# Performance work log

Hardware: AMD Instinct MI355X
Metric: run time of the kernel (lower is better)

## Reference

```python
import jax, jax.numpy as jnp
import numpy as np

B, L, NF, H = 4, 1024, 480, 32
FC = NF + H          # feat_i_classes = 512
D = FC               # downsample_feats (default None -> feat_i_classes)
W = 65               # positional window width (odd -> 'same' padding matches)
MAX0, MAX1 = 10.0, 100.0  # max_std_sigma_0 / max_std_sigma_1


def _uni(k, shape, lo=-0.01, hi=0.01):
    return jax.random.uniform(k, shape, jnp.float32, lo, hi)


def setup_inputs() -> dict:
    key = jax.random.key(0)
    ks = jax.random.split(key, 11)
    return {
        "x_embeds": jax.random.normal(ks[0], (B, L, NF), jnp.float32),
        "latent_outputs": jax.random.normal(ks[1], (B, L, H), jnp.float32),
        "masks": jnp.ones((B, L, 1), jnp.float32),
        "pos_embed": (jnp.arange(W, dtype=jnp.float32) - W // 2).reshape(W, 1, 1),
        "x": jax.random.uniform(ks[2], (B, L, 23), jnp.float32),
        "all_x_all_ampl": _uni(ks[3], (5, D, H)),
        "inp_decomp_vecs": _uni(ks[4], (5, D, 1)),
        "out_decomp_vecs": _uni(ks[5], (5, 1, H)),
        "all_x_all_bias": _uni(ks[6], (5, 1, H)),
        "pos_dep_ampl_weights": _uni(ks[7], (1, FC, H)),
        "knn_activations": _uni(ks[8], (2, FC, D)),
    }


def _conv_same(x_bdl, w_hdw):
    # torch F.conv1d (cross-correlation), stride 1, padding 'same'
    return jax.lax.conv_general_dilated(
        x_bdl, w_hdw, window_strides=(1,), padding="SAME",
        dimension_numbers=("NCH", "OIH", "NCH"))


def reference(x_embeds, latent_outputs, masks, pos_embed, x,
              all_x_all_ampl, inp_decomp_vecs, out_decomp_vecs,
              all_x_all_bias, pos_dep_ampl_weights, knn_activations):
    A = all_x_all_ampl                       # (5,D,H)
    rec = lambda i: inp_decomp_vecs[i] * out_decomp_vecs[i]  # (D,1)*(1,H)->(D,H)
    inv_c0 = 1.0 / MAX0 ** 2

    cls = jax.nn.softmax(latent_outputs * masks, axis=-1) * masks
    oef = jnp.concatenate([x_embeds, cls], axis=-1)          # (B,L,FC)
    cf0 = oef @ knn_activations[0]                           # (B,L,D)
    cf1 = oef @ knn_activations[1]                           # (B,L,D)

    def kern(ampl, mean, inv_var):
        # cos(0*pos+0)=1; pos (W,1,1) broadcast vs (D,H) -> (W,D,H)
        return jnp.exp(-inv_var * (pos_embed - mean) ** 2) * ampl

    # torch: std=abs(w)**0.5; inv_var = std**2 + 1/max0**2 = abs(w)+c
    k0 = kern(A[0], rec(0), jnp.abs(rec(1)) + inv_c0)
    k1 = kern(A[1], 0.0,    jnp.abs(rec(2)) + inv_c0)
    k2 = kern(A[2], rec(3), jnp.abs(rec(4)) + inv_c0)

    conv = lambda f, k: _conv_same(f.transpose(0, 2, 1),
                                   k.transpose(2, 1, 0)).transpose(0, 2, 1)
    acts0 = conv(cf0, k0)                                    # (B,L,H)
    acts1 = conv(cf1, k1)
    acts2 = conv(cf0, k2)

    b0, b1, b2, b3, class_mult = all_x_all_bias              # each (1,H)
    rec_dist_filt = (acts0 + b0) * acts1 \
        + acts2 * (cf1 @ A[1] + b2) \
        + (cf0 @ A[3] + b1) * (cf1 @ A[4])

    collect = jnp.sum(x[..., 21:], axis=-1, keepdims=True)   # (B,L,1)
    m = (masks + collect)[..., 0]                            # (B,L)
    pos = jnp.arange(L, dtype=jnp.float32)
    rel2 = (pos[None, :] - pos[:, None]) ** 2                # (L,L)
    sig = class_mult[0] ** 2 + 1.0 / MAX1 ** 2               # (H,)
    G = jnp.exp(-sig[:, None, None] * rel2)                  # (H,L,L)
    # V_correction[b,i,h] = m[b,i] * sum_j G[h,i,j] m[b,j]  (mask is rank-1)
    Vc = m[:, :, None] * jnp.einsum("hij,bj->bih", G, m)     # (B,L,H)

    per_pos = oef @ pos_dep_ampl_weights[0] + b3             # (B,L,H)
    return Vc * per_pos * rec_dist_filt * masks
```

## Files before the change

### kernel.cpp

```cpp
#include <hip/hip_runtime.h>
#include <hip/hip_bf16.h>

#define BB 4
#define LL 1024
#define NFE 480
#define HH 32
#define FCC 512
#define DD 512
#define WW 65
#define BL (BB*LL)
#define BLH (BL*HH)
#define LPAD 1088

typedef short bf16x8 __attribute__((ext_vector_type(8)));
typedef float f32x16 __attribute__((ext_vector_type(16)));
typedef unsigned short us8 __attribute__((ext_vector_type(8)));

__device__ inline unsigned short f2bf(float x) {
    union { float f; unsigned u; } v; v.f = x;
    unsigned r = v.u + 0x7FFFu + ((v.u >> 16) & 1u);
    return (unsigned short)(r >> 16);
}

__device__ __align__(16) unsigned short g_oefb[BL*FCC];
__device__ __align__(16) unsigned short g_knt[2*DD*FCC];
__device__ float  g_m[BL];
__device__ __align__(16) unsigned short g_fpad[2*BB*LPAD*DD];
__device__ __align__(16) unsigned short g_kb2[(size_t)3*WW*4*8*64*8];
__device__ __align__(16) unsigned short g_kbs[4*4*8*64*8];
__device__ float  g_actsp[4][3*BLH];
__device__ float  g_small[4*BLH];
__device__ float  g_gt[HH*LL];
__device__ float  g_vsum[BLH];

__global__ __launch_bounds__(256) void kprep(const float* __restrict__ x_embeds,
                                             const float* __restrict__ latent,
                                             const float* __restrict__ masks,
                                             const float* __restrict__ x,
                                             const float* __restrict__ ampl,
                                             const float* __restrict__ inp,
                                             const float* __restrict__ outv,
                                             const float* __restrict__ pos,
                                             const float* __restrict__ bias,
                                             const float* __restrict__ pdw,
                                             const float* __restrict__ knn) {
    const int bx = blockIdx.x;
    const int tid = threadIdx.x;

    if (bx < 512) {
        const int row0 = bx * 8;
        const int r    = row0 + (tid >> 5);
        const int lane = tid & 31;

        const float mask = masks[r];
        float v = latent[r*HH + lane] * mask;
        float mx = v;
        #pragma unroll
        for (int off = 16; off > 0; off >>= 1) mx = fmaxf(mx, __shfl_xor(mx, off, 32));
        float e = __expf(v - mx);
        float s = e;
        #pragma unroll
        for (int off = 16; off > 0; off >>= 1) s += __shfl_xor(s, off, 32);
        g_oefb[r*FCC + NFE + lane] = f2bf(e / s * mask);

        if (lane == 0) g_m[r] = mask + x[r*23 + 21] + x[r*23 + 22];

        for (int idx = tid; idx < 8*NFE; idx += 256) {
            int rr = idx / NFE, c = idx - rr*NFE;
            g_oefb[(row0+rr)*FCC + c] = f2bf(x_embeds[(row0+rr)*NFE + c]);
        }
    } else if (bx < 640) {
        int idx = (bx - 512) * 256 + tid;
        int fzb = idx >> 12;
        int rem = idx & 4095;
        int rowi = rem >> 6;
        int col8 = rem & 63;
        int row = (rowi < 32) ? rowi : (1024 + rowi);
        int4 z = make_int4(0,0,0,0);
        *reinterpret_cast<int4*>(&g_fpad[((size_t)fzb*LPAD + row)*DD + col8*8]) = z;
    } else if (bx < 768) {
        __shared__ unsigned short tile[64][65];
        int idx2 = bx - 640;
        const int k0 = (idx2 & 7) * 64;
        const int n0 = ((idx2 >> 3) & 7) * 64;
        const int z  = idx2 >> 6;
        const float* __restrict__ src = knn + (size_t)z*FCC*DD;
        #pragma unroll 4
        for (int i = 0; i < 16; ++i) {
            int idx = i*256 + tid;
            int kk = idx >> 6, nn = idx & 63;
            tile[kk][nn] = f2bf(src[(size_t)(k0+kk)*DD + n0+nn]);
        }
        __syncthreads();
        #pragma unroll 4
        for (int i = 0; i < 16; ++i) {
            int idx = i*256 + tid;
            int nn = idx >> 6, kk = idx & 63;
            g_knt[((size_t)z*DD + n0+nn)*FCC + k0+kk] = tile[kk][nn];
        }
    } else if (bx < 800) {
        int t = (bx - 768)*256 + tid;
        int lane = t & 63;
        int ks = (t >> 6) & 7;
        int dt = (t >> 9) & 3;
        int o  = t >> 11;
        int l31 = lane & 31, khalf = lane >> 5;
        const float* S = (o == 0) ? ampl + 1*DD*HH :
                         (o == 1) ? ampl + 3*DD*HH :
                         (o == 2) ? ampl + 4*DD*HH : pdw;
        int k0 = dt*128 + ks*16 + khalf*8;
        us8 outw;
        #pragma unroll
        for (int i = 0; i < 8; ++i) outw[i] = f2bf(S[(size_t)(k0+i)*HH + l31]);
        *reinterpret_cast<us8*>(&g_kbs[(size_t)t*8]) = outw;
    } else if (bx < 928) {
        int idx = (bx - 800) * 256 + tid;
        int h = idx / LL;
        int dist = idx - h*LL;
        float cm = bias[4*HH + h];
        float sig = cm*cm + 1e-4f;
        float dd = (float)dist;
        g_gt[idx] = __expf(-sig * dd * dd);
    } else {
        int idx3 = bx - 928;
        int xi  = idx3 & 7;
        int rem = idx3 >> 3;
        int w   = rem % 65;
        int z   = rem / 65;
        int idx = xi * 256 + tid;
        const int lane = idx & 63;
        const int ks   = (idx >> 6) & 7;
        const int dt   = idx >> 9;
        const int h    = lane & 31;
        const int d8   = dt*128 + ks*16 + (lane >> 5)*8;

        const float c0 = 0.01f;
        const float p = pos[w];
        int ai, mi, vi;
        if (z == 0)      { ai = 0; mi = 0;  vi = 1; }
        else if (z == 1) { ai = 1; mi = -1; vi = 2; }
        else             { ai = 2; mi = 3;  vi = 4; }

        us8 outw;
        #pragma unroll
        for (int i = 0; i < 8; ++i) {
            int d = d8 + i;
            float a    = ampl[(size_t)ai*DD*HH + d*HH + h];
            float mean = (mi >= 0) ? inp[mi*DD + d] * outv[mi*HH + h] : 0.f;
            float iv   = fabsf(inp[vi*DD + d] * outv[vi*HH + h]) + c0;
            float tt = p - mean;
            outw[i] = f2bf(__expf(-iv * tt * tt) * a);
        }
        *reinterpret_cast<us8*>(&g_kb2[((((size_t)z*WW + w)*4 + dt)*8 + ks)*512 + (size_t)lane*8]) = outw;
    }
}

__global__ __launch_bounds__(256) void k2_mfma() {
    const int nt = blockIdx.x;
    const int mt = blockIdx.y;
    const int z  = blockIdx.z;
    const int t  = threadIdx.x;
    const int wave = t >> 6, lane = t & 63;
    const int l31 = lane & 31, khalf = lane >> 5;
    const int n0 = nt*128 + wave*32;
    const int m_base = mt*64;

    __shared__ __align__(16) unsigned short smem[64*128];

    f32x16 acc[2];
    #pragma unroll
    for (int mti = 0; mti < 2; ++mti)
        #pragma unroll
        for (int i = 0; i < 16; ++i) acc[mti][i] = 0.f;

    const unsigned short* __restrict__ bptr =
        g_knt + ((size_t)z*DD + n0 + l31)*FCC + khalf*8;

    for (int kc = 0; kc < 4; ++kc) {
        __syncthreads();
        const unsigned short* __restrict__ src = g_oefb + (size_t)m_base*FCC + kc*128;
        #pragma unroll
        for (int c = 0; c < 4; ++c) {
            int q = c*256 + t;
            int row = q >> 4, slot = q & 15;
            int4 v = *reinterpret_cast<const int4*>(src + (size_t)row*FCC + slot*8);
            int off = row*256 + ((slot*16) ^ ((row & 15) << 4));
            *reinterpret_cast<int4*>((char*)smem + off) = v;
        }
        __syncthreads();
        #pragma unroll
        for (int ks = 0; ks < 8; ++ks) {
            bf16x8 bf = *reinterpret_cast<const bf16x8*>(bptr + kc*128 + ks*16);
            int dby = ks*32 + khalf*16;
            #pragma unroll
            for (int mti = 0; mti < 2; ++mti) {
                int r = mti*32 + l31;
                bf16x8 a = *reinterpret_cast<const bf16x8*>(
                    (char*)smem + r*256 + (dby ^ ((r & 15) << 4)));
                acc[mti] = __builtin_amdgcn_mfma_f32_32x32x16_bf16(a, bf, acc[mti], 0, 0, 0);
            }
        }
    }

    #pragma unroll
    for (int mti = 0; mti < 2; ++mti) {
        #pragma unroll
        for (int reg = 0; reg < 16; ++reg) {
            int rowf = (reg & 3) + 8*(reg >> 2) + 4*khalf;
            int m = m_base + mti*32 + rowf;
            int b_ = m >> 10, l_ = m & 1023;
            g_fpad[((size_t)(z*BB + b_)*LPAD + 32 + l_)*DD + n0 + l31] = f2bf(acc[mti][reg]);
        }
    }
}

__global__ __launch_bounds__(256) void kheavy() {
    __shared__ __align__(16) char smem_raw[32768];
    const int bx = blockIdx.x;
    const int t  = threadIdx.x;

    if (bx < 512) {
        float* ml = (float*)smem_raw;
        const int ib = bx & 127;
        const int b  = bx >> 7;
        for (int j = t; j < LL; j += 256) ml[j] = g_m[b*LL + j];
        __syncthreads();
        const int i = ib * 8 + (t & 7);
        const int h = t >> 3;
        const float* __restrict__ gt = g_gt + (size_t)h * LL;
        float a0 = 0.f, a1 = 0.f, a2 = 0.f, a3 = 0.f;
        #pragma unroll 4
        for (int j = 0; j < 256; ++j) {
            int d0 = i - j;         d0 = d0 < 0 ? -d0 : d0;
            int d1 = i - (j+256);   d1 = d1 < 0 ? -d1 : d1;
            int d2 = i - (j+512);   d2 = d2 < 0 ? -d2 : d2;
            int d3 = i - (j+768);   d3 = d3 < 0 ? -d3 : d3;
            a0 = fmaf(gt[d0], ml[j],       a0);
            a1 = fmaf(gt[d1], ml[j+256],   a1);
            a2 = fmaf(gt[d2], ml[j+512],   a2);
            a3 = fmaf(gt[d3], ml[j+768],   a3);
        }
        g_vsum[(size_t)(b*LL + i)*HH + h] = (a0 + a1) + (a2 + a3);
    } else if (bx < 1280) {
        const int g  = bx - 512;
        const int lt = g & 15;
        const int b  = (g >> 4) & 3;
        const int zdq = g >> 6;
        const int z  = zdq >> 2;
        const int dq = zdq & 3;
        const int fz = (z == 1) ? 1 : 0;
        const int wave = t >> 6, lane = t & 63;
        const int l31 = lane & 31, khalf = lane >> 5;

        const int wbeg = (wave == 0) ? 0 : 17 + (wave - 1)*16;
        const int wend = (wave == 0) ? 17 : wbeg + 16;

        f32x16 acc0, acc1;
        #pragma unroll
        for (int i = 0; i < 16; ++i) { acc0[i] = 0.f; acc1[i] = 0.f; }

        const unsigned short* src =
            g_fpad + ((size_t)(fz*BB + b)*LPAD + lt*64) * DD + dq*128;
        #pragma unroll
        for (int c = 0; c < 8; ++c) {
            int q = c*256 + t;
            int row = q >> 4, slot = q & 15;
            int4 v = *reinterpret_cast<const int4*>(src + (size_t)row*DD + slot*8);
            int off = row*256 + ((slot*16) ^ ((row & 15) << 4));
            *reinterpret_cast<int4*>(smem_raw + off) = v;
        }
        __syncthreads();

        for (int w = wbeg; w < wend; ++w) {
            const unsigned short* kbw =
                g_kb2 + ((((size_t)z*WW + w)*4 + dq)*8)*512;
            const int r0 = l31 + w;
            const int r1 = r0 + 32;
            #pragma unroll
            for (int ks = 0; ks < 8; ++ks) {
                bf16x8 bf = *reinterpret_cast<const bf16x8*>(kbw + ks*512 + lane*8);
                int dby = ks*32 + khalf*16;
                bf16x8 a0 = *reinterpret_cast<const bf16x8*>(
                    smem_raw + r0*256 + (dby ^ ((r0 & 15) << 4)));
                bf16x8 a1 = *reinterpret_cast<const bf16x8*>(
                    smem_raw + r1*256 + (dby ^ ((r1 & 15) << 4)));
                acc0 = __builtin_amdgcn_mfma_f32_32x32x16_bf16(a0, bf, acc0, 0, 0, 0);
                acc1 = __builtin_amdgcn_mfma_f32_32x32x16_bf16(a1, bf, acc1, 0, 0, 0);
            }
        }

        __syncthreads();
        float* red = (float*)smem_raw;
        #pragma unroll
        for (int reg = 0; reg < 16; ++reg) {
            int row = (reg & 3) + 8*(reg >> 2) + 4*khalf;
            red[wave*2048 + row*32 + l31]        = acc0[reg];
            red[wave*2048 + (32 + row)*32 + l31] = acc1[reg];
        }
        __syncthreads();
        float* outp = g_actsp[dq] + (size_t)z*BLH + ((size_t)b*LL + lt*64)*HH;
        #pragma unroll
        for (int j = 0; j < 8; ++j) {
            int i = j*256 + t;
            float sum = red[i] + red[2048 + i] + red[4096 + i] + red[6144 + i];
            outp[i] = sum;
        }
    } else {
        const int g = bx - 1280;
        const int mt = g & 31;
        const int o  = g >> 5;
        const int wave = t >> 6, lane = t & 63;
        const int l31 = lane & 31, khalf = lane >> 5;

        const unsigned short* src;
        if (o == 3) {
            src = g_oefb + (size_t)mt*128*FCC;
        } else {
            const int fz = (o == 1) ? 0 : 1;
            const int m0 = mt*128;
            const int b_ = m0 >> 10, l0 = m0 & 1023;
            src = g_fpad + ((size_t)(fz*BB + b_)*LPAD + 32 + l0)*DD;
        }

        f32x16 acc;
        #pragma unroll
        for (int i = 0; i < 16; ++i) acc[i] = 0.f;

        for (int kc = 0; kc < 4; ++kc) {
            __syncthreads();
            const unsigned short* s2 = src + kc*128;
            #pragma unroll
            for (int c = 0; c < 8; ++c) {
                int q = c*256 + t;
                int row = q >> 4, slot = q & 15;
                int4 v = *reinterpret_cast<const int4*>(s2 + (size_t)row*512 + slot*8);
                int off = row*256 + ((slot*16) ^ ((row & 15) << 4));
                *reinterpret_cast<int4*>(smem_raw + off) = v;
            }
            __syncthreads();
            #pragma unroll
            for (int ks = 0; ks < 8; ++ks) {
                bf16x8 bf = *reinterpret_cast<const bf16x8*>(
                    &g_kbs[((((size_t)o*4 + kc)*8 + ks)*64 + lane)*8]);
                int dby = ks*32 + khalf*16;
                int r = wave*32 + l31;
                bf16x8 a = *reinterpret_cast<const bf16x8*>(
                    smem_raw + r*256 + (dby ^ ((r & 15) << 4)));
                acc = __builtin_amdgcn_mfma_f32_32x32x16_bf16(a, bf, acc, 0, 0, 0);
            }
        }

        float* outp = g_small + (size_t)o*BLH + ((size_t)mt*128 + wave*32)*HH;
        #pragma unroll
        for (int reg = 0; reg < 16; ++reg) {
            int row = (reg & 3) + 8*(reg >> 2) + 4*khalf;
            outp[(size_t)row*HH + l31] = acc[reg];
        }
    }
}

__global__ __launch_bounds__(256) void k7_final(const float* __restrict__ masks,
                                                const float* __restrict__ bias,
                                                float* __restrict__ out) {
    int idx = blockIdx.x * 256 + threadIdx.x;
    int r = idx >> 5, h = idx & 31;
    float a0 = 0.f, a1 = 0.f, a2 = 0.f;
    #pragma unroll
    for (int s = 0; s < 4; ++s) {
        a0 += g_actsp[s][idx];
        a1 += g_actsp[s][BLH + idx];
        a2 += g_actsp[s][2*BLH + idx];
    }
    float rdf = (a0 + bias[0*HH + h]) * a1
              + a2 * (g_small[idx] + bias[2*HH + h])
              + (g_small[BLH + idx] + bias[1*HH + h]) * g_small[2*BLH + idx];
    float pp = g_small[3*BLH + idx] + bias[3*HH + h];
    float vc = g_m[r] * g_vsum[idx];
    out[idx] = vc * pp * rdf * masks[r];
}

extern "C" void kernel_launch(void* const* d_in, const int* in_sizes, int n_in,
                              void* d_out, int out_size, void* d_ws, size_t ws_size,
                              hipStream_t stream) {
    (void)in_sizes; (void)n_in; (void)d_ws; (void)ws_size; (void)out_size;
    const float* x_embeds = (const float*)d_in[0];
    const float* latent   = (const float*)d_in[1];
    const float* masks    = (const float*)d_in[2];
    const float* pos      = (const float*)d_in[3];
    const float* x        = (const float*)d_in[4];
    const float* ampl     = (const float*)d_in[5];
    const float* inp      = (const float*)d_in[6];
    const float* outv     = (const float*)d_in[7];
    const float* bias     = (const float*)d_in[8];
    const float* pdw      = (const float*)d_in[9];
    const float* knn      = (const float*)d_in[10];
    float* out = (float*)d_out;

    hipLaunchKernelGGL(kprep, dim3(2488), dim3(256), 0, stream,
                       x_embeds, latent, masks, x, ampl, inp, outv, pos, bias, pdw, knn);
    hipLaunchKernelGGL(k2_mfma, dim3(4, 64, 2), dim3(256), 0, stream);
    hipLaunchKernelGGL(kheavy, dim3(1408), dim3(256), 0, stream);
    hipLaunchKernelGGL(k7_final, dim3(BLH/256), dim3(256), 0, stream, masks, bias, out);
}
```

Before: 88.47 us.

## Window the Gaussian Vc sum, split it in halves, interleave block roles

The Vc Gaussian sum is split into two j-halves written to separate buffers, and each block only loops over j within about 512 positions of its rows. Beyond that range exp(-sig*rel^2) is negligible, since sig is at least 1/MAX1^2 by construction. Conv blocks and Vc blocks are interleaved in a 4:3 pattern within one grid so the two kinds of work share the GPU more evenly. The conv path stages only 96 feature rows in LDS and reads the second MFMA operand directly from global memory, which saves LDS traffic but adds global loads. The truncated sum drops only tiny terms, and the final kernel now adds the two partial buffers.

```diff
diff --git a/kernel.cpp b/kernel.cpp
--- a/kernel.cpp
+++ b/kernel.cpp
@@ -31,7 +31,7 @@
 __device__ float  g_actsp[4][3*BLH];
 __device__ float  g_small[4*BLH];
 __device__ float  g_gt[HH*LL];
-__device__ float  g_vsum[BLH];
+__device__ float  g_vsum2[2][BLH];
 
 __global__ __launch_bounds__(256) void kprep(const float* __restrict__ x_embeds,
                                              const float* __restrict__ latent,
@@ -219,30 +219,44 @@
     const int bx = blockIdx.x;
     const int t  = threadIdx.x;
 
-    if (bx < 512) {
+    int role, idx;
+    if (bx < 1792) {
+        int g7 = bx / 7, r7 = bx - g7*7;
+        if (r7 < 4) { role = 0; idx = g7*4 + r7; }
+        else        { role = 1; idx = g7*3 + (r7 - 4); }
+    } else { role = 2; idx = bx - 1792; }
+
+    if (role == 0) {
         float* ml = (float*)smem_raw;
-        const int ib = bx & 127;
-        const int b  = bx >> 7;
+        const int jh = idx >> 9;
+        const int rem = idx & 511;
+        const int b  = rem >> 7;
+        const int ib = rem & 127;
         for (int j = t; j < LL; j += 256) ml[j] = g_m[b*LL + j];
         __syncthreads();
         const int i = ib * 8 + (t & 7);
         const int h = t >> 3;
         const float* __restrict__ gt = g_gt + (size_t)h * LL;
+        int wlo = ib*8 - 511; int hlo = jh*512;
+        if (wlo < hlo) wlo = hlo;
+        wlo &= ~3;
+        int whi = ((ib*8 + 7 + 512) + 3) & ~3;
+        int hhi = hlo + 512;
+        if (whi > hhi) whi = hhi;
         float a0 = 0.f, a1 = 0.f, a2 = 0.f, a3 = 0.f;
-        #pragma unroll 4
-        for (int j = 0; j < 256; ++j) {
-            int d0 = i - j;         d0 = d0 < 0 ? -d0 : d0;
-            int d1 = i - (j+256);   d1 = d1 < 0 ? -d1 : d1;
-            int d2 = i - (j+512);   d2 = d2 < 0 ? -d2 : d2;
-            int d3 = i - (j+768);   d3 = d3 < 0 ? -d3 : d3;
-            a0 = fmaf(gt[d0], ml[j],       a0);
-            a1 = fmaf(gt[d1], ml[j+256],   a1);
-            a2 = fmaf(gt[d2], ml[j+512],   a2);
-            a3 = fmaf(gt[d3], ml[j+768],   a3);
-        }
-        g_vsum[(size_t)(b*LL + i)*HH + h] = (a0 + a1) + (a2 + a3);
-    } else if (bx < 1280) {
-        const int g  = bx - 512;
+        for (int j = wlo; j < whi; j += 4) {
+            int d0 = i - j;     d0 = d0 < 0 ? -d0 : d0;
+            int d1 = i - j - 1; d1 = d1 < 0 ? -d1 : d1;
+            int d2 = i - j - 2; d2 = d2 < 0 ? -d2 : d2;
+            int d3 = i - j - 3; d3 = d3 < 0 ? -d3 : d3;
+            a0 = fmaf(gt[d0], ml[j],   a0);
+            a1 = fmaf(gt[d1], ml[j+1], a1);
+            a2 = fmaf(gt[d2], ml[j+2], a2);
+            a3 = fmaf(gt[d3], ml[j+3], a3);
+        }
+        g_vsum2[jh][(size_t)(b*LL + i)*HH + h] = (a0 + a1) + (a2 + a3);
+    } else if (role == 1) {
+        const int g  = idx;
         const int lt = g & 15;
         const int b  = (g >> 4) & 3;
         const int zdq = g >> 6;
@@ -259,10 +273,10 @@
         #pragma unroll
         for (int i = 0; i < 16; ++i) { acc0[i] = 0.f; acc1[i] = 0.f; }
 
-        const unsigned short* src =
-            g_fpad + ((size_t)(fz*BB + b)*LPAD + lt*64) * DD + dq*128;
-        #pragma unroll
-        for (int c = 0; c < 8; ++c) {
+        const size_t base_row = (size_t)(fz*BB + b)*LPAD + lt*64;
+        const unsigned short* src = g_fpad + base_row * DD + dq*128;
+        #pragma unroll
+        for (int c = 0; c < 6; ++c) {
             int q = c*256 + t;
             int row = q >> 4, slot = q & 15;
             int4 v = *reinterpret_cast<const int4*>(src + (size_t)row*DD + slot*8);
@@ -271,19 +285,19 @@
         }
         __syncthreads();
 
+        const unsigned short* fb1 = src + khalf*8;
         for (int w = wbeg; w < wend; ++w) {
             const unsigned short* kbw =
                 g_kb2 + ((((size_t)z*WW + w)*4 + dq)*8)*512;
             const int r0 = l31 + w;
-            const int r1 = r0 + 32;
+            const unsigned short* fp1 = fb1 + (size_t)(r0 + 32)*DD;
             #pragma unroll
             for (int ks = 0; ks < 8; ++ks) {
                 bf16x8 bf = *reinterpret_cast<const bf16x8*>(kbw + ks*512 + lane*8);
                 int dby = ks*32 + khalf*16;
                 bf16x8 a0 = *reinterpret_cast<const bf16x8*>(
                     smem_raw + r0*256 + (dby ^ ((r0 & 15) << 4)));
-                bf16x8 a1 = *reinterpret_cast<const bf16x8*>(
-                    smem_raw + r1*256 + (dby ^ ((r1 & 15) << 4)));
+                bf16x8 a1 = *reinterpret_cast<const bf16x8*>(fp1 + ks*16);
                 acc0 = __builtin_amdgcn_mfma_f32_32x32x16_bf16(a0, bf, acc0, 0, 0, 0);
                 acc1 = __builtin_amdgcn_mfma_f32_32x32x16_bf16(a1, bf, acc1, 0, 0, 0);
             }
@@ -306,7 +320,7 @@
             outp[i] = sum;
         }
     } else {
-        const int g = bx - 1280;
+        const int g = idx;
         const int mt = g & 31;
         const int o  = g >> 5;
         const int wave = t >> 6, lane = t & 63;
@@ -375,7 +389,7 @@
               + a2 * (g_small[idx] + bias[2*HH + h])
               + (g_small[BLH + idx] + bias[1*HH + h]) * g_small[2*BLH + idx];
     float pp = g_small[3*BLH + idx] + bias[3*HH + h];
-    float vc = g_m[r] * g_vsum[idx];
+    float vc = g_m[r] * (g_vsum2[0][idx] + g_vsum2[1][idx]);
     out[idx] = vc * pp * rdf * masks[r];
 }
 
@@ -399,6 +413,6 @@
     hipLaunchKernelGGL(kprep, dim3(2488), dim3(256), 0, stream,
                        x_embeds, latent, masks, x, ampl, inp, outv, pos, bias, pdw, knn);
     hipLaunchKernelGGL(k2_mfma, dim3(4, 64, 2), dim3(256), 0, stream);
-    hipLaunchKernelGGL(kheavy, dim3(1408), dim3(256), 0, stream);
+    hipLaunchKernelGGL(kheavy, dim3(1920), dim3(256), 0, stream);
     hipLaunchKernelGGL(k7_final, dim3(BLH/256), dim3(256), 0, stream, masks, bias, out);
 }
```

Result: slower. 156.0 us (+76.4%).

## Truncate Gaussian position sum to a window and fuse cf0 convolutions

Applied to the files above, without the earlier changes.

The Gaussian-weighted mask sum now loops only over positions within about ±352 of each output row tile, using float4 loads of the shared mask, instead of all 1024 positions. The floor of 1/MAX1² on sigma bounds the dropped weights to tiny values, so the truncation is a small approximation. The two convolutions that read cf0 (kernels 0 and 2) now share one shared-memory tile load and issue MFMAs for both kernels together. The cf1 convolution gets its own block range, which cuts the block count. The fused path doubles the accumulator registers, which may lower occupancy.

```diff
diff --git a/kernel.cpp b/kernel.cpp
--- a/kernel.cpp
+++ b/kernel.cpp
@@ -228,39 +228,39 @@
         const int i = ib * 8 + (t & 7);
         const int h = t >> 3;
         const float* __restrict__ gt = g_gt + (size_t)h * LL;
+        const int i0 = ib * 8;
+        int wlo = i0 - 352; if (wlo < 0) wlo = 0; else wlo &= ~3;
+        int whi = i0 + 360; if (whi > 1024) whi = 1024; else whi = (whi + 3) & ~3;
         float a0 = 0.f, a1 = 0.f, a2 = 0.f, a3 = 0.f;
-        #pragma unroll 4
-        for (int j = 0; j < 256; ++j) {
-            int d0 = i - j;         d0 = d0 < 0 ? -d0 : d0;
-            int d1 = i - (j+256);   d1 = d1 < 0 ? -d1 : d1;
-            int d2 = i - (j+512);   d2 = d2 < 0 ? -d2 : d2;
-            int d3 = i - (j+768);   d3 = d3 < 0 ? -d3 : d3;
-            a0 = fmaf(gt[d0], ml[j],       a0);
-            a1 = fmaf(gt[d1], ml[j+256],   a1);
-            a2 = fmaf(gt[d2], ml[j+512],   a2);
-            a3 = fmaf(gt[d3], ml[j+768],   a3);
+        for (int j = wlo; j < whi; j += 4) {
+            float4 mj = *reinterpret_cast<const float4*>(&ml[j]);
+            int d0 = i - j;     d0 = d0 < 0 ? -d0 : d0;
+            int d1 = i - j - 1; d1 = d1 < 0 ? -d1 : d1;
+            int d2 = i - j - 2; d2 = d2 < 0 ? -d2 : d2;
+            int d3 = i - j - 3; d3 = d3 < 0 ? -d3 : d3;
+            a0 = fmaf(gt[d0], mj.x, a0);
+            a1 = fmaf(gt[d1], mj.y, a1);
+            a2 = fmaf(gt[d2], mj.z, a2);
+            a3 = fmaf(gt[d3], mj.w, a3);
         }
         g_vsum[(size_t)(b*LL + i)*HH + h] = (a0 + a1) + (a2 + a3);
-    } else if (bx < 1280) {
+    } else if (bx < 768) {
         const int g  = bx - 512;
         const int lt = g & 15;
         const int b  = (g >> 4) & 3;
-        const int zdq = g >> 6;
-        const int z  = zdq >> 2;
-        const int dq = zdq & 3;
-        const int fz = (z == 1) ? 1 : 0;
+        const int dq = g >> 6;
         const int wave = t >> 6, lane = t & 63;
         const int l31 = lane & 31, khalf = lane >> 5;
 
         const int wbeg = (wave == 0) ? 0 : 17 + (wave - 1)*16;
         const int wend = (wave == 0) ? 17 : wbeg + 16;
 
-        f32x16 acc0, acc1;
-        #pragma unroll
-        for (int i = 0; i < 16; ++i) { acc0[i] = 0.f; acc1[i] = 0.f; }
+        f32x16 acc00, acc01, acc20, acc21;
+        #pragma unroll
+        for (int i = 0; i < 16; ++i) { acc00[i] = 0.f; acc01[i] = 0.f; acc20[i] = 0.f; acc21[i] = 0.f; }
 
         const unsigned short* src =
-            g_fpad + ((size_t)(fz*BB + b)*LPAD + lt*64) * DD + dq*128;
+            g_fpad + ((size_t)b*LPAD + lt*64) * DD + dq*128;
         #pragma unroll
         for (int c = 0; c < 8; ++c) {
             int q = c*256 + t;
@@ -272,8 +272,84 @@
         __syncthreads();
 
         for (int w = wbeg; w < wend; ++w) {
-            const unsigned short* kbw =
-                g_kb2 + ((((size_t)z*WW + w)*4 + dq)*8)*512;
+            const unsigned short* kbw0 = g_kb2 + ((((size_t)0*WW + w)*4 + dq)*8)*512;
+            const unsigned short* kbw2 = g_kb2 + ((((size_t)2*WW + w)*4 + dq)*8)*512;
+            const int r0 = l31 + w;
+            const int r1 = r0 + 32;
+            #pragma unroll
+            for (int ks = 0; ks < 8; ++ks) {
+                bf16x8 bf0 = *reinterpret_cast<const bf16x8*>(kbw0 + ks*512 + lane*8);
+                bf16x8 bf2 = *reinterpret_cast<const bf16x8*>(kbw2 + ks*512 + lane*8);
+                int dby = ks*32 + khalf*16;
+                bf16x8 a0 = *reinterpret_cast<const bf16x8*>(
+                    smem_raw + r0*256 + (dby ^ ((r0 & 15) << 4)));
+                bf16x8 a1 = *reinterpret_cast<const bf16x8*>(
+                    smem_raw + r1*256 + (dby ^ ((r1 & 15) << 4)));
+                acc00 = __builtin_amdgcn_mfma_f32_32x32x16_bf16(a0, bf0, acc00, 0, 0, 0);
+                acc01 = __builtin_amdgcn_mfma_f32_32x32x16_bf16(a1, bf0, acc01, 0, 0, 0);
+                acc20 = __builtin_amdgcn_mfma_f32_32x32x16_bf16(a0, bf2, acc20, 0, 0, 0);
+                acc21 = __builtin_amdgcn_mfma_f32_32x32x16_bf16(a1, bf2, acc21, 0, 0, 0);
+            }
+        }
+
+        __syncthreads();
+        float* red = (float*)smem_raw;
+        #pragma unroll
+        for (int reg = 0; reg < 16; ++reg) {
+            int row = (reg & 3) + 8*(reg >> 2) + 4*khalf;
+            red[wave*2048 + row*32 + l31]        = acc00[reg];
+            red[wave*2048 + (32 + row)*32 + l31] = acc01[reg];
+        }
+        __syncthreads();
+        float* outp0 = g_actsp[dq] + ((size_t)b*LL + lt*64)*HH;
+        #pragma unroll
+        for (int j = 0; j < 8; ++j) {
+            int i = j*256 + t;
+            outp0[i] = red[i] + red[2048 + i] + red[4096 + i] + red[6144 + i];
+        }
+        __syncthreads();
+        #pragma unroll
+        for (int reg = 0; reg < 16; ++reg) {
+            int row = (reg & 3) + 8*(reg >> 2) + 4*khalf;
+            red[wave*2048 + row*32 + l31]        = acc20[reg];
+            red[wave*2048 + (32 + row)*32 + l31] = acc21[reg];
+        }
+        __syncthreads();
+        float* outp2 = g_actsp[dq] + (size_t)2*BLH + ((size_t)b*LL + lt*64)*HH;
+        #pragma unroll
+        for (int j = 0; j < 8; ++j) {
+            int i = j*256 + t;
+            outp2[i] = red[i] + red[2048 + i] + red[4096 + i] + red[6144 + i];
+        }
+    } else if (bx < 1024) {
+        const int g  = bx - 768;
+        const int lt = g & 15;
+        const int b  = (g >> 4) & 3;
+        const int dq = g >> 6;
+        const int wave = t >> 6, lane = t & 63;
+        const int l31 = lane & 31, khalf = lane >> 5;
+
+        const int wbeg = (wave == 0) ? 0 : 17 + (wave - 1)*16;
+        const int wend = (wave == 0) ? 17 : wbeg + 16;
+
+        f32x16 acc0, acc1;
+        #pragma unroll
+        for (int i = 0; i < 16; ++i) { acc0[i] = 0.f; acc1[i] = 0.f; }
+
+        const unsigned short* src =
+            g_fpad + ((size_t)(BB + b)*LPAD + lt*64) * DD + dq*128;
+        #pragma unroll
+        for (int c = 0; c < 8; ++c) {
+            int q = c*256 + t;
+            int row = q >> 4, slot = q & 15;
+            int4 v = *reinterpret_cast<const int4*>(src + (size_t)row*DD + slot*8);
+            int off = row*256 + ((slot*16) ^ ((row & 15) << 4));
+            *reinterpret_cast<int4*>(smem_raw + off) = v;
+        }
+        __syncthreads();
+
+        for (int w = wbeg; w < wend; ++w) {
+            const unsigned short* kbw = g_kb2 + ((((size_t)1*WW + w)*4 + dq)*8)*512;
             const int r0 = l31 + w;
             const int r1 = r0 + 32;
             #pragma unroll
@@ -298,15 +374,14 @@
             red[wave*2048 + (32 + row)*32 + l31] = acc1[reg];
         }
         __syncthreads();
-        float* outp = g_actsp[dq] + (size_t)z*BLH + ((size_t)b*LL + lt*64)*HH;
+        float* outp = g_actsp[dq] + (size_t)BLH + ((size_t)b*LL + lt*64)*HH;
         #pragma unroll
         for (int j = 0; j < 8; ++j) {
             int i = j*256 + t;
-            float sum = red[i] + red[2048 + i] + red[4096 + i] + red[6144 + i];
-            outp[i] = sum;
+            outp[i] = red[i] + red[2048 + i] + red[4096 + i] + red[6144 + i];
         }
     } else {
-        const int g = bx - 1280;
+        const int g = bx - 1024;
         const int mt = g & 31;
         const int o  = g >> 5;
         const int wave = t >> 6, lane = t & 63;
@@ -399,6 +474,6 @@
     hipLaunchKernelGGL(kprep, dim3(2488), dim3(256), 0, stream,
                        x_embeds, latent, masks, x, ampl, inp, outv, pos, bias, pdw, knn);
     hipLaunchKernelGGL(k2_mfma, dim3(4, 64, 2), dim3(256), 0, stream);
-    hipLaunchKernelGGL(kheavy, dim3(1408), dim3(256), 0, stream);
+    hipLaunchKernelGGL(kheavy, dim3(1152), dim3(256), 0, stream);
     hipLaunchKernelGGL(k7_final, dim3(BLH/256), dim3(256), 0, stream, masks, bias, out);
 }
```

Result: slower. 93.83 us (+6.1%).

## Truncate Gaussian position sum to a finite window and split it across blocks

Applied to the files above, without the earlier changes.

The dense per-position Gaussian sum over all 1024 positions is limited to a ±352 window around each output tile. This relies on the kernel width never falling below the 1e-4 floor, so far-away terms are negligible. The Gaussian table is transposed to distance-major with h innermost, so lanes that differ in h read adjacent addresses, and mask values are loaded as float4. The window is split into two halves run by separate blocks, with the final kernel adding the two partial sums. This trades a small truncation error, an extra buffer and more blocks for much less arithmetic and more parallelism.

```diff
diff --git a/kernel.cpp b/kernel.cpp
--- a/kernel.cpp
+++ b/kernel.cpp
@@ -31,7 +31,7 @@
 __device__ float  g_actsp[4][3*BLH];
 __device__ float  g_small[4*BLH];
 __device__ float  g_gt[HH*LL];
-__device__ float  g_vsum[BLH];
+__device__ float  g_vsum2[2][BLH];
 
 __global__ __launch_bounds__(256) void kprep(const float* __restrict__ x_embeds,
                                              const float* __restrict__ latent,
@@ -115,8 +115,8 @@
         *reinterpret_cast<us8*>(&g_kbs[(size_t)t*8]) = outw;
     } else if (bx < 928) {
         int idx = (bx - 800) * 256 + tid;
-        int h = idx / LL;
-        int dist = idx - h*LL;
+        int h = idx & 31;
+        int dist = idx >> 5;
         float cm = bias[4*HH + h];
         float sig = cm*cm + 1e-4f;
         float dd = (float)dist;
@@ -219,30 +219,8 @@
     const int bx = blockIdx.x;
     const int t  = threadIdx.x;
 
-    if (bx < 512) {
-        float* ml = (float*)smem_raw;
-        const int ib = bx & 127;
-        const int b  = bx >> 7;
-        for (int j = t; j < LL; j += 256) ml[j] = g_m[b*LL + j];
-        __syncthreads();
-        const int i = ib * 8 + (t & 7);
-        const int h = t >> 3;
-        const float* __restrict__ gt = g_gt + (size_t)h * LL;
-        float a0 = 0.f, a1 = 0.f, a2 = 0.f, a3 = 0.f;
-        #pragma unroll 4
-        for (int j = 0; j < 256; ++j) {
-            int d0 = i - j;         d0 = d0 < 0 ? -d0 : d0;
-            int d1 = i - (j+256);   d1 = d1 < 0 ? -d1 : d1;
-            int d2 = i - (j+512);   d2 = d2 < 0 ? -d2 : d2;
-            int d3 = i - (j+768);   d3 = d3 < 0 ? -d3 : d3;
-            a0 = fmaf(gt[d0], ml[j],       a0);
-            a1 = fmaf(gt[d1], ml[j+256],   a1);
-            a2 = fmaf(gt[d2], ml[j+512],   a2);
-            a3 = fmaf(gt[d3], ml[j+768],   a3);
-        }
-        g_vsum[(size_t)(b*LL + i)*HH + h] = (a0 + a1) + (a2 + a3);
-    } else if (bx < 1280) {
-        const int g  = bx - 512;
+    if (bx < 768) {
+        const int g  = bx;
         const int lt = g & 15;
         const int b  = (g >> 4) & 3;
         const int zdq = g >> 6;
@@ -305,8 +283,40 @@
             float sum = red[i] + red[2048 + i] + red[4096 + i] + red[6144 + i];
             outp[i] = sum;
         }
+    } else if (bx < 1792) {
+        float* ml = (float*)smem_raw;
+        const int g  = bx - 768;
+        const int jh = g >> 9;
+        const int rem = g & 511;
+        const int b  = rem >> 7;
+        const int ib = rem & 127;
+        for (int j = t; j < LL; j += 256) ml[j] = g_m[b*LL + j];
+        __syncthreads();
+        const int h = t & 31;
+        const int i = ib * 8 + (t >> 5);
+        const float* __restrict__ gtt = g_gt;
+        const int i0 = ib * 8;
+        int wlo = i0 - 352; if (wlo < 0) wlo = 0; else wlo &= ~3;
+        int whi = i0 + 360; if (whi > 1024) whi = 1024; else whi = (whi + 3) & ~3;
+        int wmid = wlo + ((((whi - wlo) >> 1) + 3) & ~3);
+        if (wmid > whi) wmid = whi;
+        const int jlo = jh ? wmid : wlo;
+        const int jhi = jh ? whi : wmid;
+        float a0 = 0.f, a1 = 0.f, a2 = 0.f, a3 = 0.f;
+        for (int j = jlo; j < jhi; j += 4) {
+            float4 mj = *reinterpret_cast<const float4*>(&ml[j]);
+            int d0 = i - j;     d0 = d0 < 0 ? -d0 : d0;
+            int d1 = i - j - 1; d1 = d1 < 0 ? -d1 : d1;
+            int d2 = i - j - 2; d2 = d2 < 0 ? -d2 : d2;
+            int d3 = i - j - 3; d3 = d3 < 0 ? -d3 : d3;
+            a0 = fmaf(gtt[d0*HH + h], mj.x, a0);
+            a1 = fmaf(gtt[d1*HH + h], mj.y, a1);
+            a2 = fmaf(gtt[d2*HH + h], mj.z, a2);
+            a3 = fmaf(gtt[d3*HH + h], mj.w, a3);
+        }
+        g_vsum2[jh][(size_t)(b*LL + i)*HH + h] = (a0 + a1) + (a2 + a3);
     } else {
-        const int g = bx - 1280;
+        const int g = bx - 1792;
         const int mt = g & 31;
         const int o  = g >> 5;
         const int wave = t >> 6, lane = t & 63;
@@ -375,7 +385,7 @@
               + a2 * (g_small[idx] + bias[2*HH + h])
               + (g_small[BLH + idx] + bias[1*HH + h]) * g_small[2*BLH + idx];
     float pp = g_small[3*BLH + idx] + bias[3*HH + h];
-    float vc = g_m[r] * g_vsum[idx];
+    float vc = g_m[r] * (g_vsum2[0][idx] + g_vsum2[1][idx]);
     out[idx] = vc * pp * rdf * masks[r];
 }
 
@@ -399,6 +409,6 @@
     hipLaunchKernelGGL(kprep, dim3(2488), dim3(256), 0, stream,
                        x_embeds, latent, masks, x, ampl, inp, outv, pos, bias, pdw, knn);
     hipLaunchKernelGGL(k2_mfma, dim3(4, 64, 2), dim3(256), 0, stream);
-    hipLaunchKernelGGL(kheavy, dim3(1408), dim3(256), 0, stream);
+    hipLaunchKernelGGL(kheavy, dim3(1920), dim3(256), 0, stream);
     hipLaunchKernelGGL(k7_final, dim3(BLH/256), dim3(256), 0, stream, masks, bias, out);
 }
```

After: 86.16 us. -2.6%, faster.
